# Kernel tuning notes

Measured on AMD Instinct MI355X. Metric: run time of the kernel, lower is better.

## Reference

```python
import jax, jax.numpy as jnp
import numpy as np

B, T, D = 2, 2048, 1024
H = 16
HD = D // H  # 64


def _rope_tables(t_len, hd, dtype=jnp.float32):
    inv_freq = 1.0 / (10000.0 ** (jnp.arange(0, hd, 2, dtype=jnp.float32) / hd))
    freqs = jnp.outer(jnp.arange(t_len, dtype=jnp.float32), inv_freq)  # [T, hd/2]
    emb = jnp.concatenate([freqs, freqs], axis=-1)  # [T, hd]
    return emb.astype(dtype)


def _rotate_half(x):
    x1, x2 = jnp.split(x, 2, axis=-1)
    return jnp.concatenate([-x2, x1], axis=-1)


def setup_inputs() -> dict:
    key = jax.random.key(0)
    k1, k2, k3 = jax.random.split(key, 3)
    x = jax.random.normal(k1, (B, T, D), dtype=jnp.float32)
    w_qkv = jax.random.normal(k2, (D, 3 * D), dtype=jnp.float32) * (D ** -0.5)
    w_out = jax.random.normal(k3, (D, D), dtype=jnp.float32) * (D ** -0.5)
    return {"x": x, "w_qkv": w_qkv, "w_out": w_out}


def reference(x, w_qkv, w_out):
    Bc, Tc, Dc = x.shape
    scale = HD ** -0.5
    qkv = x @ w_qkv  # [B,T,3D]
    q, k, v = jnp.split(qkv, 3, axis=-1)
    # -> [B,H,T,hd]
    q = q.reshape(Bc, Tc, H, HD).transpose(0, 2, 1, 3)
    k = k.reshape(Bc, Tc, H, HD).transpose(0, 2, 1, 3)
    v = v.reshape(Bc, Tc, H, HD).transpose(0, 2, 1, 3)
    emb = _rope_tables(Tc, HD, x.dtype)  # [T,hd]
    cos = jnp.cos(emb)[None, None, :, :]
    sin = jnp.sin(emb)[None, None, :, :]
    q = q * cos + _rotate_half(q) * sin
    k = k * cos + _rotate_half(k) * sin
    attn = jnp.einsum('bhqd,bhkd->bhqk', q, k) * scale  # [B,H,T,T]
    causal = jnp.tril(jnp.ones((Tc, Tc), dtype=bool))
    attn = jnp.where(causal[None, None], attn, -jnp.inf)
    attn = jax.nn.softmax(attn, axis=-1)
    out = jnp.einsum('bhqk,bhkd->bhqd', attn, v)
    out = out.transpose(0, 2, 1, 3).reshape(Bc, Tc, Dc)
    return out @ w_out
```

## Files before the change

### kernel.cpp

```cpp
#include <hip/hip_runtime.h>

#define TSEQ 2048
#define DMODEL 1024
#define NHEAD 16
#define HDIM 64
#define NB 2
#define MROWS 4096
#define NQKV 3072
#define QSCALE 0.1803368801111204f
#define ROPE_C (13.2877123795494f / 32.0f)
#define NEGINF -3.0e38f

using s16x8 = __attribute__((ext_vector_type(8))) short;
using s16x4 = __attribute__((ext_vector_type(4))) short;
using f32x4 = __attribute__((ext_vector_type(4))) float;
using u32x2 = __attribute__((ext_vector_type(2))) unsigned int;

static __device__ __forceinline__ float b2f(unsigned short u) {
  union { unsigned int i; float f; } x; x.i = ((unsigned int)u) << 16; return x.f;
}
static __device__ __forceinline__ unsigned short f2b(float f) {
  unsigned int u = __float_as_uint(f);
  u += 0x7fffu + ((u >> 16) & 1u);
  return (unsigned short)(u >> 16);
}

#if __has_builtin(__builtin_amdgcn_exp2f)
#define EXP2(x) __builtin_amdgcn_exp2f(x)
#else
#define EXP2(x) exp2f(x)
#endif

typedef const __attribute__((address_space(1))) char gchar;
typedef __attribute__((address_space(3))) char lchar;
static __device__ __forceinline__ void gload_lds16(const void* g, void* l) {
  __builtin_amdgcn_global_load_lds((gchar*)g, (lchar*)l, 16, 0, 0);
}

__global__ __launch_bounds__(256) void k_prep(const float* __restrict__ x,
                                              short* __restrict__ xb,
                                              const float* __restrict__ wq,
                                              short* __restrict__ wqT,
                                              const float* __restrict__ wo,
                                              short* __restrict__ woT) {
  __shared__ float tile[32][33];
  const int blk = blockIdx.x;
  const int tid = threadIdx.x;
  if (blk < 4096) {
    const int i = blk * 256 + tid;
    const float4 v = ((const float4*)x)[i];
    s16x4 o;
    o.x = (short)f2b(v.x); o.y = (short)f2b(v.y);
    o.z = (short)f2b(v.z); o.w = (short)f2b(v.w);
    ((s16x4*)xb)[i] = o;
    return;
  }
  const float* in; short* out; int C, bx, by;
  if (blk < 7168) {
    const int l = blk - 4096; in = wq; out = wqT; C = NQKV;
    bx = l % 96; by = l / 96;
  } else {
    const int l = blk - 7168; in = wo; out = woT; C = DMODEL;
    bx = l & 31; by = l >> 5;
  }
  const int tx = tid & 31, ty4 = (tid >> 5) * 4;
#pragma unroll
  for (int i = 0; i < 4; ++i)
    tile[ty4 + i][tx] = in[(by * 32 + ty4 + i) * C + bx * 32 + tx];
  __syncthreads();
#pragma unroll
  for (int i = 0; i < 4; ++i)
    out[(bx * 32 + ty4 + i) * DMODEL + by * 32 + tx] = (short)f2b(tile[tx][ty4 + i]);
}

__global__ __launch_bounds__(256) void k_gemm_qkv(const short* __restrict__ A,
                                                  const short* __restrict__ BT,
                                                  short* __restrict__ Qo,
                                                  short* __restrict__ Ko,
                                                  short* __restrict__ Vt) {
  __shared__ __attribute__((aligned(16))) short As[2][128 * 64];
  __shared__ __attribute__((aligned(16))) short Bs[2][128 * 64];
  const int K = DMODEL;
  const int tid = threadIdx.x;
  const int wave = tid >> 6, lane = tid & 63, quad = lane >> 4, l15 = lane & 15;
  const int wm = (wave >> 1) * 64, wn = (wave & 1) * 64;
  const int m0 = blockIdx.y * 128, n0 = blockIdx.x * 128;
  f32x4 acc[4][4] = {};
  const char* Ab = (const char*)A;
  const char* Bb = (const char*)BT;
  char* AsB = (char*)As;
  char* BsB = (char*)Bs;
  int srow[4], sg[4];
#pragma unroll
  for (int p = 0; p < 4; ++p) {
    const int i = p * 256 + tid;
    srow[p] = i >> 3;
    sg[p] = (i & 7) ^ (srow[p] & 7);
  }
#define QSTAGE(k0v, buf)                                                     \
  do {                                                                       \
    _Pragma("unroll")                                                        \
    for (int p = 0; p < 4; ++p) {                                            \
      const long goA = ((long)(m0 + srow[p]) * K + (k0v)) * 2 + sg[p] * 16;  \
      gload_lds16(Ab + goA, AsB + (buf) * 16384 + p * 4096 + wave * 1024);   \
      const long goB = ((long)(n0 + srow[p]) * K + (k0v)) * 2 + sg[p] * 16;  \
      gload_lds16(Bb + goB, BsB + (buf) * 16384 + p * 4096 + wave * 1024);   \
    }                                                                        \
  } while (0)

  const int nK = K / 64;
  QSTAGE(0, 0);
  for (int kt = 0; kt < nK; ++kt) {
    const int cur = kt & 1;
    if (kt + 1 < nK) {
      QSTAGE((kt + 1) * 64, cur ^ 1);
      asm volatile("s_waitcnt vmcnt(8)" ::: "memory");
    } else {
      asm volatile("s_waitcnt vmcnt(0)" ::: "memory");
    }
    __builtin_amdgcn_s_barrier();
    const char* Ac = AsB + cur * 16384;
    const char* Bc = BsB + cur * 16384;
#pragma unroll
    for (int hf = 0; hf < 2; ++hf) {
      s16x8 af[4], bf[4];
#pragma unroll
      for (int i = 0; i < 4; ++i) {
        const int ra = wm + i * 16 + l15;
        af[i] = *(const s16x8*)(Ac + ra * 128 + (((hf * 4 + quad) ^ (ra & 7)) * 16));
        const int rb = wn + i * 16 + l15;
        bf[i] = *(const s16x8*)(Bc + rb * 128 + (((hf * 4 + quad) ^ (rb & 7)) * 16));
      }
#pragma unroll
      for (int i = 0; i < 4; ++i)
#pragma unroll
        for (int j = 0; j < 4; ++j)
          acc[i][j] = __builtin_amdgcn_mfma_f32_16x16x32_bf16(af[i], bf[j], acc[i][j], 0, 0, 0);
    }
    asm volatile("s_waitcnt lgkmcnt(0)" ::: "memory");
    __builtin_amdgcn_s_barrier();
  }
#undef QSTAGE
  const int colbase = n0 + wn;
  const int region = colbase >> 10;
  const int hh = (colbase & 1023) >> 6;
  const int bq = m0 >> 11;
  const int tbase = (m0 & 2047) + wm;
  char* sw = (char*)As + wave * 8192;
  if (region == 2) {
#pragma unroll
    for (int i = 0; i < 4; ++i)
#pragma unroll
      for (int j = 0; j < 4; ++j) {
        const int d = j * 16 + l15;
        const int t0 = i * 16 + quad * 4;
        s16x4 w;
        w.x = (short)f2b(acc[i][j][0]);
        w.y = (short)f2b(acc[i][j][1]);
        w.z = (short)f2b(acc[i][j][2]);
        w.w = (short)f2b(acc[i][j][3]);
        *(s16x4*)(sw + d * 128 + ((((t0 >> 3) ^ (d & 7))) * 16) + (t0 & 7) * 2) = w;
      }
    short* dstv = Vt + (((long)(bq * NHEAD + hh) * HDIM) << 11);
#pragma unroll
    for (int p = 0; p < 8; ++p) {
      const int linear = p * 64 + lane;
      const int d = linear >> 3, c = linear & 7;
      const s16x8 v = *(const s16x8*)(sw + d * 128 + ((c ^ (d & 7)) * 16));
      *(s16x8*)(dstv + (((long)d) << 11) + tbase + c * 8) = v;
    }
  } else {
    if (region == 1) {
#pragma unroll
      for (int i = 0; i < 4; ++i)
#pragma unroll
        for (int j = 0; j < 2; ++j) {
          const int d = j * 16 + l15;
          const float inv = exp2f(-(float)d * ROPE_C);
#pragma unroll
          for (int r = 0; r < 4; ++r) {
            const int t = tbase + i * 16 + quad * 4 + r;
            float sn, cs;
            __sincosf((float)t * inv, &sn, &cs);
            const float a = acc[i][j][r];
            const float bv = acc[i][j + 2][r];
            acc[i][j][r]     = a * cs - bv * sn;
            acc[i][j + 2][r] = bv * cs + a * sn;
          }
        }
    }
#pragma unroll
    for (int i = 0; i < 4; ++i)
#pragma unroll
      for (int j = 0; j < 4; ++j)
#pragma unroll
        for (int r = 0; r < 4; ++r) {
          const int row = i * 16 + quad * 4 + r;
          const int col = j * 16 + l15;
          *(short*)(sw + row * 128 + ((((col >> 3) ^ (row & 7))) * 16) + (col & 7) * 2)
              = (short)f2b(acc[i][j][r]);
        }
    short* dst = (region ? Ko : Qo) + ((long)(bq * NHEAD + hh) * TSEQ + tbase) * HDIM;
#pragma unroll
    for (int p = 0; p < 8; ++p) {
      const int linear = p * 64 + lane;
      const int r = linear >> 3, c = linear & 7;
      const s16x8 v = *(const s16x8*)(sw + r * 128 + ((c ^ (r & 7)) * 16));
      *(s16x8*)(dst + (long)r * HDIM + c * 8) = v;
    }
  }
}

template <int IM, bool OUT_BF16>
__global__ __launch_bounds__(256) void k_gemm(const short* __restrict__ A,
                                              const short* __restrict__ BT,
                                              void* __restrict__ Cv,
                                              int M, int N, int K) {
  static_assert(IM == 2, "vmcnt literal assumes IM==2 (6 loads/thread)");
  __shared__ __attribute__((aligned(16))) short As[2][IM * 32 * 64];
  __shared__ __attribute__((aligned(16))) short Bs[2][128 * 64];
  const int tid = threadIdx.x;
  const int wave = tid >> 6, lane = tid & 63, quad = lane >> 4, l15 = lane & 15;
  const int wm = (wave >> 1) * (IM * 16), wn = (wave & 1) * 64;
  const int m0 = blockIdx.y * (IM * 32), n0 = blockIdx.x * 128;
  f32x4 acc[IM][4] = {};
  const char* Ab = (const char*)A;
  const char* Bb = (const char*)BT;
  char* AsB = (char*)As;
  char* BsB = (char*)Bs;
  int srow[4], sg[4];
#pragma unroll
  for (int p = 0; p < 4; ++p) {
    const int i = p * 256 + tid;
    srow[p] = i >> 3;
    sg[p] = (i & 7) ^ (srow[p] & 7);
  }
#define GSTAGE(k0v, buf)                                                       \
  do {                                                                         \
    _Pragma("unroll")                                                          \
    for (int p = 0; p < IM; ++p) {                                             \
      const long go = ((long)(m0 + srow[p]) * K + (k0v)) * 2 + sg[p] * 16;     \
      gload_lds16(Ab + go, AsB + (buf) * (IM * 4096) + p * 4096 + wave * 1024);\
    }                                                                          \
    _Pragma("unroll")                                                          \
    for (int p = 0; p < 4; ++p) {                                              \
      const long go = ((long)(n0 + srow[p]) * K + (k0v)) * 2 + sg[p] * 16;     \
      gload_lds16(Bb + go, BsB + (buf) * 16384 + p * 4096 + wave * 1024);      \
    }                                                                          \
  } while (0)

  const int nK = K / 64;
  GSTAGE(0, 0);
  for (int kt = 0; kt < nK; ++kt) {
    const int cur = kt & 1;
    if (kt + 1 < nK) {
      GSTAGE((kt + 1) * 64, cur ^ 1);
      asm volatile("s_waitcnt vmcnt(6)" ::: "memory");
    } else {
      asm volatile("s_waitcnt vmcnt(0)" ::: "memory");
    }
    __builtin_amdgcn_s_barrier();
    const char* Ac = AsB + cur * (IM * 4096);
    const char* Bc = BsB + cur * 16384;
#pragma unroll
    for (int hf = 0; hf < 2; ++hf) {
      s16x8 af[IM], bf[4];
#pragma unroll
      for (int i = 0; i < IM; ++i) {
        const int ra = wm + i * 16 + l15;
        af[i] = *(const s16x8*)(Ac + ra * 128 + (((hf * 4 + quad) ^ (ra & 7)) * 16));
      }
#pragma unroll
      for (int j = 0; j < 4; ++j) {
        const int rb = wn + j * 16 + l15;
        bf[j] = *(const s16x8*)(Bc + rb * 128 + (((hf * 4 + quad) ^ (rb & 7)) * 16));
      }
#pragma unroll
      for (int i = 0; i < IM; ++i)
#pragma unroll
        for (int j = 0; j < 4; ++j)
          acc[i][j] = __builtin_amdgcn_mfma_f32_16x16x32_bf16(af[i], bf[j], acc[i][j], 0, 0, 0);
    }
    asm volatile("s_waitcnt lgkmcnt(0)" ::: "memory");
    __builtin_amdgcn_s_barrier();
  }
#undef GSTAGE
  if (OUT_BF16) {
#pragma unroll
    for (int i = 0; i < IM; ++i) {
      const int row = m0 + wm + i * 16 + quad * 4;
#pragma unroll
      for (int j = 0; j < 4; ++j) {
        const int col = n0 + wn + j * 16 + l15;
#pragma unroll
        for (int r = 0; r < 4; ++r)
          ((short*)Cv)[(long)(row + r) * N + col] = (short)f2b(acc[i][j][r]);
      }
    }
  } else {
    char* sw = (char*)Bs + wave * 8192;
#pragma unroll
    for (int i = 0; i < IM; ++i)
#pragma unroll
      for (int j = 0; j < 4; ++j)
#pragma unroll
        for (int r = 0; r < 4; ++r) {
          const int row = i * 16 + quad * 4 + r;
          const int col = j * 16 + l15;
          *(float*)(sw + row * 256 + ((((col >> 2) ^ (row & 7))) * 16) + (col & 3) * 4)
              = acc[i][j][r];
        }
    float* C = (float*)Cv;
#pragma unroll
    for (int p = 0; p < 8; ++p) {
      const int linear = p * 64 + lane;
      const int r = linear >> 4, c = linear & 15;
      const f32x4 v = *(const f32x4*)(sw + r * 256 + ((c ^ (r & 7)) * 16));
      *(f32x4*)(C + (long)(m0 + wm + r) * N + n0 + wn + c * 4) = v;
    }
  }
}

__global__ __launch_bounds__(512) __attribute__((amdgpu_waves_per_eu(4)))
void k_attn(const short* __restrict__ Qg,
            const short* __restrict__ Kg,
            const short* __restrict__ Vg,
            short* __restrict__ O) {
  __shared__ __attribute__((aligned(16))) short Ks[2][64 * 64];
  __shared__ __attribute__((aligned(16))) short Vs[2][64 * 64];
  __shared__ __attribute__((aligned(16))) short pl[8][16 * 64];
  const int bx = blockIdx.x, by = blockIdx.y;
  const int qi = ((by >> 4) & 1) ? (15 - bx) : bx;
  const int bh = by;
  const int b = bh >> 4, h = bh & 15;
  const int tid = threadIdx.x, wave = tid >> 6, lane = tid & 63;
  const int quad = lane >> 4, l15 = lane & 15;
  const char* Kb = (const char*)(Kg + (long)bh * TSEQ * HDIM);
  const char* Vb = (const char*)(Vg + (long)bh * HDIM * TSEQ);
  const short* Qb = Qg + (long)bh * TSEQ * HDIM;
  const int qr0 = qi * 128 + wave * 16;
  const s16x8 rq0 = *(const s16x8*)&Qb[(qr0 + l15) * HDIM + quad * 8];
  const s16x8 rq1 = *(const s16x8*)&Qb[(qr0 + l15) * HDIM + 32 + quad * 8];
  s16x8 aq0, aq1;
  {
    const float tf = (float)(qr0 + l15);
#pragma unroll
    for (int j = 0; j < 8; ++j) {
      const float inv = exp2f(-(float)(quad * 8 + j) * ROPE_C);
      float sn, cs;
      __sincosf(tf * inv, &sn, &cs);
      sn *= QSCALE; cs *= QSCALE;
      const float q0 = b2f((unsigned short)rq0[j]);
      const float q1 = b2f((unsigned short)rq1[j]);
      aq0[j] = (short)f2b(q0 * cs - q1 * sn);
      aq1[j] = (short)f2b(q1 * cs + q0 * sn);
    }
  }
  s16x8 ones;
#pragma unroll
  for (int j = 0; j < 8; ++j) ones[j] = (short)0x3F80;
  f32x4 o[4] = {};
  f32x4 zs = {};
  const int kr0 = tid >> 3, kg0 = (tid & 7) ^ (kr0 & 7);
  char* KsB = (char*)Ks;
  char* VsB = (char*)Vs;
  char* plwB = (char*)pl + wave * 2048;
  const int ldsw = wave * 1024;

#define STAGE(kjv, buf)                                                     \
  do {                                                                      \
    gload_lds16(Kb + (kjv) * 8192 + (kr0 * 8 + kg0) * 16,                   \
                KsB + (buf) * 8192 + ldsw);                                 \
    gload_lds16(Vb + (kjv) * 128 + kr0 * (TSEQ * 2) + kg0 * 16,             \
                VsB + (buf) * 8192 + ldsw);                                 \
  } while (0)

  STAGE(0, 0);

  const int kjmax = 2 * qi + 1;
  const int kjd = qr0 >> 6;
  for (int kj = 0; kj <= kjmax; ++kj) {
    const int cur = kj & 1;
    if (kj < kjmax) {
      STAGE(kj + 1, cur ^ 1);
      asm volatile("s_waitcnt vmcnt(2)" ::: "memory");
    } else {
      asm volatile("s_waitcnt vmcnt(0)" ::: "memory");
    }
    __builtin_amdgcn_s_barrier();
    if (kj <= kjd) {
      const char* kb = KsB + cur * 8192;
      const char* vb = VsB + cur * 8192;
      f32x4 s[4];
      __builtin_amdgcn_s_setprio(1);
#pragma unroll
      for (int j2 = 0; j2 < 4; ++j2) {
        const int row = j2 * 16 + l15;
        const s16x8 k0 = *(const s16x8*)(kb + row * 128 + ((quad ^ (row & 7)) * 16));
        const s16x8 k1 = *(const s16x8*)(kb + row * 128 + (((4 + quad) ^ (row & 7)) * 16));
        f32x4 z = {};
        z = __builtin_amdgcn_mfma_f32_16x16x32_bf16(k0, aq0, z, 0, 0, 0);
        z = __builtin_amdgcn_mfma_f32_16x16x32_bf16(k1, aq1, z, 0, 0, 0);
        s[j2] = z;
      }
      __builtin_amdgcn_s_setprio(0);
      if (kj == kjd) {
        const int qloc = (qr0 & 63) + l15;
#pragma unroll
        for (int j2 = 0; j2 < 4; ++j2)
#pragma unroll
          for (int r = 0; r < 4; ++r)
            if (j2 * 16 + quad * 4 + r > qloc) s[j2][r] = NEGINF;
      }
#pragma unroll
      for (int j2 = 0; j2 < 4; ++j2) {
        const unsigned int u0 = __float_as_uint(EXP2(s[j2][0])) & 0xffff0000u;
        const unsigned int u1 = __float_as_uint(EXP2(s[j2][1])) & 0xffff0000u;
        const unsigned int u2 = __float_as_uint(EXP2(s[j2][2])) & 0xffff0000u;
        const unsigned int u3 = __float_as_uint(EXP2(s[j2][3])) & 0xffff0000u;
        u32x2 w;
        w.x = (u0 >> 16) | u1;
        w.y = (u2 >> 16) | u3;
        const int t0 = j2 * 16 + quad * 4;
        *(u32x2*)(plwB + l15 * 128 + (((t0 >> 3) ^ (l15 & 7)) * 16) + (quad & 1) * 8) = w;
      }
      const s16x8 bp0 = *(const s16x8*)(plwB + l15 * 128 + ((quad ^ (l15 & 7)) * 16));
      const s16x8 bp1 = *(const s16x8*)(plwB + l15 * 128 + (((4 + quad) ^ (l15 & 7)) * 16));
      __builtin_amdgcn_s_setprio(1);
      zs = __builtin_amdgcn_mfma_f32_16x16x32_bf16(ones, bp0, zs, 0, 0, 0);
      zs = __builtin_amdgcn_mfma_f32_16x16x32_bf16(ones, bp1, zs, 0, 0, 0);
#pragma unroll
      for (int hs = 0; hs < 4; ++hs) {
        const int d = hs * 16 + l15;
        const s16x8 av0 = *(const s16x8*)(vb + d * 128 + ((quad ^ (d & 7)) * 16));
        const s16x8 av1 = *(const s16x8*)(vb + d * 128 + (((4 + quad) ^ (d & 7)) * 16));
        o[hs] = __builtin_amdgcn_mfma_f32_16x16x32_bf16(av0, bp0, o[hs], 0, 0, 0);
        o[hs] = __builtin_amdgcn_mfma_f32_16x16x32_bf16(av1, bp1, o[hs], 0, 0, 0);
      }
      __builtin_amdgcn_s_setprio(0);
    }
    asm volatile("s_waitcnt lgkmcnt(0)" ::: "memory");
    __builtin_amdgcn_s_barrier();
  }
#undef STAGE
  const float rinv = 1.0f / zs[0];
  const int t = qr0 + l15;
  short* Orow = O + (long)(b * TSEQ + t) * DMODEL + h * HDIM + quad * 4;
#pragma unroll
  for (int hs = 0; hs < 4; ++hs) {
    s16x4 w;
    w.x = (short)f2b(o[hs][0] * rinv);
    w.y = (short)f2b(o[hs][1] * rinv);
    w.z = (short)f2b(o[hs][2] * rinv);
    w.w = (short)f2b(o[hs][3] * rinv);
    *(s16x4*)(Orow + hs * 16) = w;
  }
}

extern "C" void kernel_launch(void* const* d_in, const int* in_sizes, int n_in,
                              void* d_out, int out_size, void* d_ws, size_t ws_size,
                              hipStream_t stream) {
  const float* x = (const float*)d_in[0];
  const float* w_qkv = (const float*)d_in[1];
  const float* w_out = (const float*)d_in[2];
  float* out = (float*)d_out;
  char* ws = (char*)d_ws;

  short* xb    = (short*)(ws);
  short* wqkvT = (short*)(ws + (8ll << 20));
  short* woutT = (short*)(ws + (14ll << 20));
  short* Qb    = (short*)(ws + (16ll << 20));
  short* Kb    = (short*)(ws + (24ll << 20));
  short* Vt    = (short*)(ws + (32ll << 20));
  short* Ob    = (short*)(ws + (40ll << 20));

  k_prep<<<dim3(8192), dim3(256), 0, stream>>>(x, xb, w_qkv, wqkvT, w_out, woutT);
  k_gemm_qkv<<<dim3(NQKV / 128, MROWS / 128), dim3(256), 0, stream>>>(
      xb, wqkvT, Qb, Kb, Vt);
  k_attn<<<dim3(TSEQ / 128, NB * NHEAD), dim3(512), 0, stream>>>(Qb, Kb, Vt, Ob);
  k_gemm<2, false><<<dim3(DMODEL / 128, MROWS / 64), dim3(256), 0, stream>>>(
      Ob, woutT, (void*)out, MROWS, DMODEL, DMODEL);
}
```

Measured before the change: 178.5 us.

## Process two query sub-tiles per wave in attention and swizzle GEMM block order

The attention kernel now runs 4 waves of 256 threads instead of 8, and each wave handles 32 query rows as two 16-row sub-tiles. Every K/V fragment read from LDS feeds twice as many MFMAs, and each thread issues twice as many staging loads. Both GEMMs also remap block IDs with an XCD-style swizzle so neighbouring tiles land on the same chiplet and share L2. The costs are higher register pressure from doubled accumulators, fewer waves to hide latency, and no explicit waves_per_eu hint.

```diff
diff --git a/kernel.cpp b/kernel.cpp
--- a/kernel.cpp
+++ b/kernel.cpp
@@ -84,7 +84,10 @@
   const int tid = threadIdx.x;
   const int wave = tid >> 6, lane = tid & 63, quad = lane >> 4, l15 = lane & 15;
   const int wm = (wave >> 1) * 64, wn = (wave & 1) * 64;
-  const int m0 = blockIdx.y * 128, n0 = blockIdx.x * 128;
+  const int bid = blockIdx.y * 24 + blockIdx.x;
+  const int swz = (bid & 7) * 96 + (bid >> 3);
+  const int bx = swz % 24, by = swz / 24;
+  const int m0 = by * 128, n0 = bx * 128;
   f32x4 acc[4][4] = {};
   const char* Ab = (const char*)A;
   const char* Bb = (const char*)BT;
@@ -222,7 +225,11 @@
   const int tid = threadIdx.x;
   const int wave = tid >> 6, lane = tid & 63, quad = lane >> 4, l15 = lane & 15;
   const int wm = (wave >> 1) * (IM * 16), wn = (wave & 1) * 64;
-  const int m0 = blockIdx.y * (IM * 32), n0 = blockIdx.x * 128;
+  const int nwg = gridDim.x * gridDim.y;
+  const int bid = blockIdx.y * gridDim.x + blockIdx.x;
+  const int swz = (bid & 7) * (nwg >> 3) + (bid >> 3);
+  const int bx = swz % gridDim.x, by = swz / gridDim.x;
+  const int m0 = by * (IM * 32), n0 = bx * 128;
   f32x4 acc[IM][4] = {};
   const char* Ab = (const char*)A;
   const char* Bb = (const char*)BT;
@@ -321,14 +328,49 @@
   }
 }
 
-__global__ __launch_bounds__(512) __attribute__((amdgpu_waves_per_eu(4)))
-void k_attn(const short* __restrict__ Qg,
-            const short* __restrict__ Kg,
-            const short* __restrict__ Vg,
-            short* __restrict__ O) {
+static __device__ __forceinline__ void load_rope_q(const short* Qb, int row,
+                                                   int quad, s16x8* a0, s16x8* a1) {
+  const s16x8 r0 = *(const s16x8*)&Qb[row * HDIM + quad * 8];
+  const s16x8 r1 = *(const s16x8*)&Qb[row * HDIM + 32 + quad * 8];
+  const float tf = (float)row;
+  s16x8 o0, o1;
+#pragma unroll
+  for (int j = 0; j < 8; ++j) {
+    const float inv = exp2f(-(float)(quad * 8 + j) * ROPE_C);
+    float sn, cs;
+    __sincosf(tf * inv, &sn, &cs);
+    sn *= QSCALE; cs *= QSCALE;
+    const float q0 = b2f((unsigned short)r0[j]);
+    const float q1 = b2f((unsigned short)r1[j]);
+    o0[j] = (short)f2b(q0 * cs - q1 * sn);
+    o1[j] = (short)f2b(q1 * cs + q0 * sn);
+  }
+  *a0 = o0; *a1 = o1;
+}
+
+static __device__ __forceinline__ void pexp_store(char* plw, const f32x4* s,
+                                                  int quad, int l15) {
+#pragma unroll
+  for (int j2 = 0; j2 < 4; ++j2) {
+    const unsigned int u0 = __float_as_uint(EXP2(s[j2][0])) & 0xffff0000u;
+    const unsigned int u1 = __float_as_uint(EXP2(s[j2][1])) & 0xffff0000u;
+    const unsigned int u2 = __float_as_uint(EXP2(s[j2][2])) & 0xffff0000u;
+    const unsigned int u3 = __float_as_uint(EXP2(s[j2][3])) & 0xffff0000u;
+    u32x2 w;
+    w.x = (u0 >> 16) | u1;
+    w.y = (u2 >> 16) | u3;
+    const int t0 = j2 * 16 + quad * 4;
+    *(u32x2*)(plw + l15 * 128 + (((t0 >> 3) ^ (l15 & 7)) * 16) + (quad & 1) * 8) = w;
+  }
+}
+
+__global__ __launch_bounds__(256) void k_attn(const short* __restrict__ Qg,
+                                              const short* __restrict__ Kg,
+                                              const short* __restrict__ Vg,
+                                              short* __restrict__ O) {
   __shared__ __attribute__((aligned(16))) short Ks[2][64 * 64];
   __shared__ __attribute__((aligned(16))) short Vs[2][64 * 64];
-  __shared__ __attribute__((aligned(16))) short pl[8][16 * 64];
+  __shared__ __attribute__((aligned(16))) short pl[4][2][16 * 64];
   const int bx = blockIdx.x, by = blockIdx.y;
   const int qi = ((by >> 4) & 1) ? (15 - bx) : bx;
   const int bh = by;
@@ -338,41 +380,34 @@
   const char* Kb = (const char*)(Kg + (long)bh * TSEQ * HDIM);
   const char* Vb = (const char*)(Vg + (long)bh * HDIM * TSEQ);
   const short* Qb = Qg + (long)bh * TSEQ * HDIM;
-  const int qr0 = qi * 128 + wave * 16;
-  const s16x8 rq0 = *(const s16x8*)&Qb[(qr0 + l15) * HDIM + quad * 8];
-  const s16x8 rq1 = *(const s16x8*)&Qb[(qr0 + l15) * HDIM + 32 + quad * 8];
-  s16x8 aq0, aq1;
-  {
-    const float tf = (float)(qr0 + l15);
-#pragma unroll
-    for (int j = 0; j < 8; ++j) {
-      const float inv = exp2f(-(float)(quad * 8 + j) * ROPE_C);
-      float sn, cs;
-      __sincosf(tf * inv, &sn, &cs);
-      sn *= QSCALE; cs *= QSCALE;
-      const float q0 = b2f((unsigned short)rq0[j]);
-      const float q1 = b2f((unsigned short)rq1[j]);
-      aq0[j] = (short)f2b(q0 * cs - q1 * sn);
-      aq1[j] = (short)f2b(q1 * cs + q0 * sn);
-    }
-  }
+  const int qr0 = qi * 128 + wave * 32;
+
+  s16x8 aqA0, aqA1, aqB0, aqB1;
+  load_rope_q(Qb, qr0 + l15, quad, &aqA0, &aqA1);
+  load_rope_q(Qb, qr0 + 16 + l15, quad, &aqB0, &aqB1);
+
   s16x8 ones;
 #pragma unroll
   for (int j = 0; j < 8; ++j) ones[j] = (short)0x3F80;
-  f32x4 o[4] = {};
-  f32x4 zs = {};
-  const int kr0 = tid >> 3, kg0 = (tid & 7) ^ (kr0 & 7);
+  f32x4 oA[4] = {}, oB[4] = {}, zsA = {}, zsB = {};
   char* KsB = (char*)Ks;
   char* VsB = (char*)Vs;
-  char* plwB = (char*)pl + wave * 2048;
+  char* plA = (char*)pl + wave * 4096;
+  char* plB = plA + 2048;
+  const int r0 = tid >> 3,        g0 = (tid & 7) ^ (r0 & 7);
+  const int r1 = 32 + (tid >> 3), g1 = (tid & 7) ^ (r1 & 7);
   const int ldsw = wave * 1024;
 
 #define STAGE(kjv, buf)                                                     \
   do {                                                                      \
-    gload_lds16(Kb + (kjv) * 8192 + (kr0 * 8 + kg0) * 16,                   \
+    gload_lds16(Kb + (kjv) * 8192 + (r0 * 8 + g0) * 16,                     \
                 KsB + (buf) * 8192 + ldsw);                                 \
-    gload_lds16(Vb + (kjv) * 128 + kr0 * (TSEQ * 2) + kg0 * 16,             \
+    gload_lds16(Kb + (kjv) * 8192 + (r1 * 8 + g1) * 16,                     \
+                KsB + (buf) * 8192 + 4096 + ldsw);                          \
+    gload_lds16(Vb + (kjv) * 128 + r0 * (TSEQ * 2) + g0 * 16,               \
                 VsB + (buf) * 8192 + ldsw);                                 \
+    gload_lds16(Vb + (kjv) * 128 + r1 * (TSEQ * 2) + g1 * 16,               \
+                VsB + (buf) * 8192 + 4096 + ldsw);                          \
   } while (0)
 
   STAGE(0, 0);
@@ -383,7 +418,7 @@
     const int cur = kj & 1;
     if (kj < kjmax) {
       STAGE(kj + 1, cur ^ 1);
-      asm volatile("s_waitcnt vmcnt(2)" ::: "memory");
+      asm volatile("s_waitcnt vmcnt(4)" ::: "memory");
     } else {
       asm volatile("s_waitcnt vmcnt(0)" ::: "memory");
     }
@@ -391,7 +426,7 @@
     if (kj <= kjd) {
       const char* kb = KsB + cur * 8192;
       const char* vb = VsB + cur * 8192;
-      f32x4 s[4];
+      f32x4 sA[4], sB[4];
       __builtin_amdgcn_s_setprio(1);
 #pragma unroll
       for (int j2 = 0; j2 < 4; ++j2) {
@@ -399,43 +434,46 @@
         const s16x8 k0 = *(const s16x8*)(kb + row * 128 + ((quad ^ (row & 7)) * 16));
         const s16x8 k1 = *(const s16x8*)(kb + row * 128 + (((4 + quad) ^ (row & 7)) * 16));
         f32x4 z = {};
-        z = __builtin_amdgcn_mfma_f32_16x16x32_bf16(k0, aq0, z, 0, 0, 0);
-        z = __builtin_amdgcn_mfma_f32_16x16x32_bf16(k1, aq1, z, 0, 0, 0);
-        s[j2] = z;
+        z = __builtin_amdgcn_mfma_f32_16x16x32_bf16(k0, aqA0, z, 0, 0, 0);
+        z = __builtin_amdgcn_mfma_f32_16x16x32_bf16(k1, aqA1, z, 0, 0, 0);
+        sA[j2] = z;
+        f32x4 y = {};
+        y = __builtin_amdgcn_mfma_f32_16x16x32_bf16(k0, aqB0, y, 0, 0, 0);
+        y = __builtin_amdgcn_mfma_f32_16x16x32_bf16(k1, aqB1, y, 0, 0, 0);
+        sB[j2] = y;
       }
       __builtin_amdgcn_s_setprio(0);
       if (kj == kjd) {
-        const int qloc = (qr0 & 63) + l15;
+        const int qA = (qr0 & 63) + l15;
 #pragma unroll
         for (int j2 = 0; j2 < 4; ++j2)
 #pragma unroll
-          for (int r = 0; r < 4; ++r)
-            if (j2 * 16 + quad * 4 + r > qloc) s[j2][r] = NEGINF;
-      }
-#pragma unroll
-      for (int j2 = 0; j2 < 4; ++j2) {
-        const unsigned int u0 = __float_as_uint(EXP2(s[j2][0])) & 0xffff0000u;
-        const unsigned int u1 = __float_as_uint(EXP2(s[j2][1])) & 0xffff0000u;
-        const unsigned int u2 = __float_as_uint(EXP2(s[j2][2])) & 0xffff0000u;
-        const unsigned int u3 = __float_as_uint(EXP2(s[j2][3])) & 0xffff0000u;
-        u32x2 w;
-        w.x = (u0 >> 16) | u1;
-        w.y = (u2 >> 16) | u3;
-        const int t0 = j2 * 16 + quad * 4;
-        *(u32x2*)(plwB + l15 * 128 + (((t0 >> 3) ^ (l15 & 7)) * 16) + (quad & 1) * 8) = w;
-      }
-      const s16x8 bp0 = *(const s16x8*)(plwB + l15 * 128 + ((quad ^ (l15 & 7)) * 16));
-      const s16x8 bp1 = *(const s16x8*)(plwB + l15 * 128 + (((4 + quad) ^ (l15 & 7)) * 16));
+          for (int r = 0; r < 4; ++r) {
+            const int tl = j2 * 16 + quad * 4 + r;
+            if (tl > qA) sA[j2][r] = NEGINF;
+            if (tl > qA + 16) sB[j2][r] = NEGINF;
+          }
+      }
+      pexp_store(plA, sA, quad, l15);
+      pexp_store(plB, sB, quad, l15);
+      const s16x8 bpA0 = *(const s16x8*)(plA + l15 * 128 + ((quad ^ (l15 & 7)) * 16));
+      const s16x8 bpA1 = *(const s16x8*)(plA + l15 * 128 + (((4 + quad) ^ (l15 & 7)) * 16));
+      const s16x8 bpB0 = *(const s16x8*)(plB + l15 * 128 + ((quad ^ (l15 & 7)) * 16));
+      const s16x8 bpB1 = *(const s16x8*)(plB + l15 * 128 + (((4 + quad) ^ (l15 & 7)) * 16));
       __builtin_amdgcn_s_setprio(1);
-      zs = __builtin_amdgcn_mfma_f32_16x16x32_bf16(ones, bp0, zs, 0, 0, 0);
-      zs = __builtin_amdgcn_mfma_f32_16x16x32_bf16(ones, bp1, zs, 0, 0, 0);
+      zsA = __builtin_amdgcn_mfma_f32_16x16x32_bf16(ones, bpA0, zsA, 0, 0, 0);
+      zsA = __builtin_amdgcn_mfma_f32_16x16x32_bf16(ones, bpA1, zsA, 0, 0, 0);
+      zsB = __builtin_amdgcn_mfma_f32_16x16x32_bf16(ones, bpB0, zsB, 0, 0, 0);
+      zsB = __builtin_amdgcn_mfma_f32_16x16x32_bf16(ones, bpB1, zsB, 0, 0, 0);
 #pragma unroll
       for (int hs = 0; hs < 4; ++hs) {
         const int d = hs * 16 + l15;
         const s16x8 av0 = *(const s16x8*)(vb + d * 128 + ((quad ^ (d & 7)) * 16));
         const s16x8 av1 = *(const s16x8*)(vb + d * 128 + (((4 + quad) ^ (d & 7)) * 16));
-        o[hs] = __builtin_amdgcn_mfma_f32_16x16x32_bf16(av0, bp0, o[hs], 0, 0, 0);
-        o[hs] = __builtin_amdgcn_mfma_f32_16x16x32_bf16(av1, bp1, o[hs], 0, 0, 0);
+        oA[hs] = __builtin_amdgcn_mfma_f32_16x16x32_bf16(av0, bpA0, oA[hs], 0, 0, 0);
+        oA[hs] = __builtin_amdgcn_mfma_f32_16x16x32_bf16(av1, bpA1, oA[hs], 0, 0, 0);
+        oB[hs] = __builtin_amdgcn_mfma_f32_16x16x32_bf16(av0, bpB0, oB[hs], 0, 0, 0);
+        oB[hs] = __builtin_amdgcn_mfma_f32_16x16x32_bf16(av1, bpB1, oB[hs], 0, 0, 0);
       }
       __builtin_amdgcn_s_setprio(0);
     }
@@ -443,17 +481,33 @@
     __builtin_amdgcn_s_barrier();
   }
 #undef STAGE
-  const float rinv = 1.0f / zs[0];
-  const int t = qr0 + l15;
-  short* Orow = O + (long)(b * TSEQ + t) * DMODEL + h * HDIM + quad * 4;
-#pragma unroll
-  for (int hs = 0; hs < 4; ++hs) {
-    s16x4 w;
-    w.x = (short)f2b(o[hs][0] * rinv);
-    w.y = (short)f2b(o[hs][1] * rinv);
-    w.z = (short)f2b(o[hs][2] * rinv);
-    w.w = (short)f2b(o[hs][3] * rinv);
-    *(s16x4*)(Orow + hs * 16) = w;
+  const float rA = 1.0f / zsA[0];
+  const float rB = 1.0f / zsB[0];
+  {
+    const int t = qr0 + l15;
+    short* Orow = O + (long)(b * TSEQ + t) * DMODEL + h * HDIM + quad * 4;
+#pragma unroll
+    for (int hs = 0; hs < 4; ++hs) {
+      s16x4 w;
+      w.x = (short)f2b(oA[hs][0] * rA);
+      w.y = (short)f2b(oA[hs][1] * rA);
+      w.z = (short)f2b(oA[hs][2] * rA);
+      w.w = (short)f2b(oA[hs][3] * rA);
+      *(s16x4*)(Orow + hs * 16) = w;
+    }
+  }
+  {
+    const int t = qr0 + 16 + l15;
+    short* Orow = O + (long)(b * TSEQ + t) * DMODEL + h * HDIM + quad * 4;
+#pragma unroll
+    for (int hs = 0; hs < 4; ++hs) {
+      s16x4 w;
+      w.x = (short)f2b(oB[hs][0] * rB);
+      w.y = (short)f2b(oB[hs][1] * rB);
+      w.z = (short)f2b(oB[hs][2] * rB);
+      w.w = (short)f2b(oB[hs][3] * rB);
+      *(s16x4*)(Orow + hs * 16) = w;
+    }
   }
 }
 
@@ -477,7 +531,7 @@
   k_prep<<<dim3(8192), dim3(256), 0, stream>>>(x, xb, w_qkv, wqkvT, w_out, woutT);
   k_gemm_qkv<<<dim3(NQKV / 128, MROWS / 128), dim3(256), 0, stream>>>(
       xb, wqkvT, Qb, Kb, Vt);
-  k_attn<<<dim3(TSEQ / 128, NB * NHEAD), dim3(512), 0, stream>>>(Qb, Kb, Vt, Ob);
+  k_attn<<<dim3(TSEQ / 128, NB * NHEAD), dim3(256), 0, stream>>>(Qb, Kb, Vt, Ob);
   k_gemm<2, false><<<dim3(DMODEL / 128, MROWS / 64), dim3(256), 0, stream>>>(
       Ob, woutT, (void*)out, MROWS, DMODEL, DMODEL);
 }
```

After: 187.8 us. 5.2% more time.

## Stage QKV GEMM tiles through registers, single LDS buffer, and XCD-swizzle workgroups

Applied to the files above, without the earlier changes.

The QKV GEMM drops the double-buffered direct global-to-LDS loads. It prefetches the next K-tile into registers, then writes it to a single swizzled LDS buffer after the MFMA work, adding an extra barrier per iteration. This halves LDS use to allow more occupancy, but adds register pressure and an extra sync. Both GEMM kernels also remap block IDs with a stride-8 swizzle so neighbouring tiles land on the same XCD, aiming for better L2 reuse.

```diff
diff --git a/kernel.cpp b/kernel.cpp
--- a/kernel.cpp
+++ b/kernel.cpp
@@ -78,58 +78,62 @@
                                                   short* __restrict__ Qo,
                                                   short* __restrict__ Ko,
                                                   short* __restrict__ Vt) {
-  __shared__ __attribute__((aligned(16))) short As[2][128 * 64];
-  __shared__ __attribute__((aligned(16))) short Bs[2][128 * 64];
+  __shared__ __attribute__((aligned(16))) short As[128 * 64];
+  __shared__ __attribute__((aligned(16))) short Bs[128 * 64];
   const int K = DMODEL;
   const int tid = threadIdx.x;
   const int wave = tid >> 6, lane = tid & 63, quad = lane >> 4, l15 = lane & 15;
   const int wm = (wave >> 1) * 64, wn = (wave & 1) * 64;
-  const int m0 = blockIdx.y * 128, n0 = blockIdx.x * 128;
+  const int bid = blockIdx.y * 24 + blockIdx.x;
+  const int swz = (bid & 7) * 96 + (bid >> 3);
+  const int bx = swz % 24, by = swz / 24;
+  const int m0 = by * 128, n0 = bx * 128;
   f32x4 acc[4][4] = {};
   const char* Ab = (const char*)A;
   const char* Bb = (const char*)BT;
   char* AsB = (char*)As;
   char* BsB = (char*)Bs;
-  int srow[4], sg[4];
+  int srow[4], scg[4], ssw[4];
 #pragma unroll
   for (int p = 0; p < 4; ++p) {
     const int i = p * 256 + tid;
     srow[p] = i >> 3;
-    sg[p] = (i & 7) ^ (srow[p] & 7);
-  }
-#define QSTAGE(k0v, buf)                                                     \
-  do {                                                                       \
-    _Pragma("unroll")                                                        \
-    for (int p = 0; p < 4; ++p) {                                            \
-      const long goA = ((long)(m0 + srow[p]) * K + (k0v)) * 2 + sg[p] * 16;  \
-      gload_lds16(Ab + goA, AsB + (buf) * 16384 + p * 4096 + wave * 1024);   \
-      const long goB = ((long)(n0 + srow[p]) * K + (k0v)) * 2 + sg[p] * 16;  \
-      gload_lds16(Bb + goB, BsB + (buf) * 16384 + p * 4096 + wave * 1024);   \
-    }                                                                        \
+    scg[p] = i & 7;
+    ssw[p] = scg[p] ^ (srow[p] & 7);
+  }
+#define QLOAD(k0v)                                                            \
+  do {                                                                        \
+    _Pragma("unroll")                                                         \
+    for (int p = 0; p < 4; ++p) {                                             \
+      ra[p] = *(const f32x4*)(Ab + ((long)(m0 + srow[p]) * K + (k0v)) * 2 + scg[p] * 16); \
+      rb[p] = *(const f32x4*)(Bb + ((long)(n0 + srow[p]) * K + (k0v)) * 2 + scg[p] * 16); \
+    }                                                                         \
   } while (0)
-
+#define QWRITE()                                                              \
+  do {                                                                        \
+    _Pragma("unroll")                                                         \
+    for (int p = 0; p < 4; ++p) {                                             \
+      *(f32x4*)(AsB + srow[p] * 128 + ssw[p] * 16) = ra[p];                   \
+      *(f32x4*)(BsB + srow[p] * 128 + ssw[p] * 16) = rb[p];                   \
+    }                                                                         \
+  } while (0)
+
+  f32x4 ra[4], rb[4];
   const int nK = K / 64;
-  QSTAGE(0, 0);
+  QLOAD(0);
+  QWRITE();
+  __syncthreads();
   for (int kt = 0; kt < nK; ++kt) {
-    const int cur = kt & 1;
-    if (kt + 1 < nK) {
-      QSTAGE((kt + 1) * 64, cur ^ 1);
-      asm volatile("s_waitcnt vmcnt(8)" ::: "memory");
-    } else {
-      asm volatile("s_waitcnt vmcnt(0)" ::: "memory");
-    }
-    __builtin_amdgcn_s_barrier();
-    const char* Ac = AsB + cur * 16384;
-    const char* Bc = BsB + cur * 16384;
+    if (kt + 1 < nK) QLOAD((kt + 1) * 64);
 #pragma unroll
     for (int hf = 0; hf < 2; ++hf) {
       s16x8 af[4], bf[4];
 #pragma unroll
       for (int i = 0; i < 4; ++i) {
-        const int ra = wm + i * 16 + l15;
-        af[i] = *(const s16x8*)(Ac + ra * 128 + (((hf * 4 + quad) ^ (ra & 7)) * 16));
-        const int rb = wn + i * 16 + l15;
-        bf[i] = *(const s16x8*)(Bc + rb * 128 + (((hf * 4 + quad) ^ (rb & 7)) * 16));
+        const int rowa = wm + i * 16 + l15;
+        af[i] = *(const s16x8*)(AsB + rowa * 128 + (((hf * 4 + quad) ^ (rowa & 7)) * 16));
+        const int rowb = wn + i * 16 + l15;
+        bf[i] = *(const s16x8*)(BsB + rowb * 128 + (((hf * 4 + quad) ^ (rowb & 7)) * 16));
       }
 #pragma unroll
       for (int i = 0; i < 4; ++i)
@@ -139,14 +143,20 @@
     }
     asm volatile("s_waitcnt lgkmcnt(0)" ::: "memory");
     __builtin_amdgcn_s_barrier();
-  }
-#undef QSTAGE
+    if (kt + 1 < nK) {
+      QWRITE();
+      asm volatile("s_waitcnt lgkmcnt(0)" ::: "memory");
+      __builtin_amdgcn_s_barrier();
+    }
+  }
+#undef QLOAD
+#undef QWRITE
   const int colbase = n0 + wn;
   const int region = colbase >> 10;
   const int hh = (colbase & 1023) >> 6;
   const int bq = m0 >> 11;
   const int tbase = (m0 & 2047) + wm;
-  char* sw = (char*)As + wave * 8192;
+  char* sw = (wave < 2) ? (AsB + wave * 8192) : (BsB + (wave - 2) * 8192);
   if (region == 2) {
 #pragma unroll
     for (int i = 0; i < 4; ++i)
@@ -222,7 +232,11 @@
   const int tid = threadIdx.x;
   const int wave = tid >> 6, lane = tid & 63, quad = lane >> 4, l15 = lane & 15;
   const int wm = (wave >> 1) * (IM * 16), wn = (wave & 1) * 64;
-  const int m0 = blockIdx.y * (IM * 32), n0 = blockIdx.x * 128;
+  const int nwg = gridDim.x * gridDim.y;
+  const int bid = blockIdx.y * gridDim.x + blockIdx.x;
+  const int swz = (bid & 7) * (nwg >> 3) + (bid >> 3);
+  const int bx = swz % gridDim.x, by = swz / gridDim.x;
+  const int m0 = by * (IM * 32), n0 = bx * 128;
   f32x4 acc[IM][4] = {};
   const char* Ab = (const char*)A;
   const char* Bb = (const char*)BT;
@@ -267,13 +281,13 @@
       s16x8 af[IM], bf[4];
 #pragma unroll
       for (int i = 0; i < IM; ++i) {
-        const int ra = wm + i * 16 + l15;
-        af[i] = *(const s16x8*)(Ac + ra * 128 + (((hf * 4 + quad) ^ (ra & 7)) * 16));
+        const int rowa = wm + i * 16 + l15;
+        af[i] = *(const s16x8*)(Ac + rowa * 128 + (((hf * 4 + quad) ^ (rowa & 7)) * 16));
       }
 #pragma unroll
       for (int j = 0; j < 4; ++j) {
-        const int rb = wn + j * 16 + l15;
-        bf[j] = *(const s16x8*)(Bc + rb * 128 + (((hf * 4 + quad) ^ (rb & 7)) * 16));
+        const int rowb = wn + j * 16 + l15;
+        bf[j] = *(const s16x8*)(Bc + rowb * 128 + (((hf * 4 + quad) ^ (rowb & 7)) * 16));
       }
 #pragma unroll
       for (int i = 0; i < IM; ++i)
```

Result: no change. 176.2 us (median of 2 runs) (-1.3%).

## Enlarge QKV GEMM to 256x256 tiles with 8 waves, phased staging, and block swizzle

Applied to the files above, without the earlier changes.

Rewrites the QKV projection GEMM to use 256x256 output tiles with 512 threads (8 waves, 2x4 layout). Each wave now holds 128x64 of the output, and global-to-LDS staging for the next K-tile is split into four phases interleaved with MFMA work, using s_setprio to favour the matrix ops. A grouped block-index swizzle is added to both the QKV GEMM and the output-projection GEMM to improve L2 reuse. The larger tile cuts redundant global loads per FLOP, at the cost of 128KB of LDS, more accumulator registers, more barriers per K step, and only 192 blocks for the QKV GEMM.

```diff
diff --git a/kernel.cpp b/kernel.cpp
--- a/kernel.cpp
+++ b/kernel.cpp
@@ -73,140 +73,176 @@
     out[(bx * 32 + ty4 + i) * DMODEL + by * 32 + tx] = (short)f2b(tile[tx][ty4 + i]);
 }
 
-__global__ __launch_bounds__(256) void k_gemm_qkv(const short* __restrict__ A,
-                                                  const short* __restrict__ BT,
-                                                  short* __restrict__ Qo,
-                                                  short* __restrict__ Ko,
-                                                  short* __restrict__ Vt) {
-  __shared__ __attribute__((aligned(16))) short As[2][128 * 64];
-  __shared__ __attribute__((aligned(16))) short Bs[2][128 * 64];
+__global__ __launch_bounds__(512, 2) void k_gemm_qkv(const short* __restrict__ A,
+                                                     const short* __restrict__ BT,
+                                                     short* __restrict__ Qo,
+                                                     short* __restrict__ Ko,
+                                                     short* __restrict__ Vt) {
+  __shared__ __attribute__((aligned(16))) short L[2][2][2][128 * 64];
   const int K = DMODEL;
   const int tid = threadIdx.x;
   const int wave = tid >> 6, lane = tid & 63, quad = lane >> 4, l15 = lane & 15;
-  const int wm = (wave >> 1) * 64, wn = (wave & 1) * 64;
-  const int m0 = blockIdx.y * 128, n0 = blockIdx.x * 128;
-  f32x4 acc[4][4] = {};
-  const char* Ab = (const char*)A;
-  const char* Bb = (const char*)BT;
-  char* AsB = (char*)As;
-  char* BsB = (char*)Bs;
-  int srow[4], sg[4];
-#pragma unroll
-  for (int p = 0; p < 4; ++p) {
-    const int i = p * 256 + tid;
-    srow[p] = i >> 3;
-    sg[p] = (i & 7) ^ (srow[p] & 7);
-  }
-#define QSTAGE(k0v, buf)                                                     \
-  do {                                                                       \
-    _Pragma("unroll")                                                        \
-    for (int p = 0; p < 4; ++p) {                                            \
-      const long goA = ((long)(m0 + srow[p]) * K + (k0v)) * 2 + sg[p] * 16;  \
-      gload_lds16(Ab + goA, AsB + (buf) * 16384 + p * 4096 + wave * 1024);   \
-      const long goB = ((long)(n0 + srow[p]) * K + (k0v)) * 2 + sg[p] * 16;  \
-      gload_lds16(Bb + goB, BsB + (buf) * 16384 + p * 4096 + wave * 1024);   \
-    }                                                                        \
+  const int wr = wave >> 2, wc = wave & 3;
+  const int bid = blockIdx.y * 12 + blockIdx.x;
+  const int swz = (bid & 7) * 24 + (bid >> 3);
+  const int bx = swz % 12, by = swz / 12;
+  const int m0 = by * 256, n0 = bx * 256;
+  f32x4 acc[8][4] = {};
+  char* Lb = (char*)L;
+  const int r0 = tid >> 3, pc = tid & 7;
+  const int sc0 = pc ^ (r0 & 7);
+  const int r1 = 64 + r0;
+  const int sc1 = pc ^ (r1 & 7);
+#define HBASE(buf, ab, h) (Lb + (((buf) * 4 + (ab) * 2 + (h)) * 16384))
+#define STAGE_HT(kt1, ab, h)                                                   \
+  do {                                                                         \
+    const short* src_ = (ab) ? BT : A;                                         \
+    const int rowb_ = ((ab) ? n0 : m0) + (h) * 128;                            \
+    const long o0_ = ((long)(rowb_ + r0) * K + (kt1) * 64) * 2 + sc0 * 16;     \
+    const long o1_ = ((long)(rowb_ + r1) * K + (kt1) * 64) * 2 + sc1 * 16;     \
+    char* db_ = HBASE((kt1) & 1, ab, h) + wave * 1024;                         \
+    gload_lds16((const char*)src_ + o0_, db_);                                 \
+    gload_lds16((const char*)src_ + o1_, db_ + 8192);                          \
   } while (0)
 
-  const int nK = K / 64;
-  QSTAGE(0, 0);
-  for (int kt = 0; kt < nK; ++kt) {
+  const int nT = K / 64;
+  STAGE_HT(0, 0, 0); STAGE_HT(0, 0, 1); STAGE_HT(0, 1, 0); STAGE_HT(0, 1, 1);
+
+  const int rbb = (wc & 1) * 64;
+  for (int kt = 0; kt < nT; ++kt) {
     const int cur = kt & 1;
-    if (kt + 1 < nK) {
-      QSTAGE((kt + 1) * 64, cur ^ 1);
-      asm volatile("s_waitcnt vmcnt(8)" ::: "memory");
+    const char* Ah = HBASE(cur, 0, wr);
+    const char* Bh = HBASE(cur, 1, wc >> 1);
+    s16x8 bf[4][2];
+#pragma unroll
+    for (int ph = 0; ph < 4; ++ph) {
+      s16x8 af[2][2];
+      if (ph == 0) {
+        if (kt + 1 < nT) {
+          STAGE_HT(kt + 1, 0, 0);
+          asm volatile("s_waitcnt vmcnt(2)" ::: "memory");
+        } else {
+          asm volatile("s_waitcnt vmcnt(0)" ::: "memory");
+        }
+        __builtin_amdgcn_s_barrier();
+#pragma unroll
+        for (int g = 0; g < 4; ++g)
+#pragma unroll
+          for (int kh = 0; kh < 2; ++kh) {
+            const int rb = rbb + g * 16 + l15;
+            bf[g][kh] = *(const s16x8*)(Bh + rb * 128 +
+                                        (((kh * 4 + quad) ^ (l15 & 7)) * 16));
+          }
+#pragma unroll
+        for (int f2 = 0; f2 < 2; ++f2)
+#pragma unroll
+          for (int kh = 0; kh < 2; ++kh) {
+            const int ra = (ph * 2 + f2) * 16 + l15;
+            af[f2][kh] = *(const s16x8*)(Ah + ra * 128 +
+                                         (((kh * 4 + quad) ^ (l15 & 7)) * 16));
+          }
+      } else {
+#pragma unroll
+        for (int f2 = 0; f2 < 2; ++f2)
+#pragma unroll
+          for (int kh = 0; kh < 2; ++kh) {
+            const int ra = (ph * 2 + f2) * 16 + l15;
+            af[f2][kh] = *(const s16x8*)(Ah + ra * 128 +
+                                         (((kh * 4 + quad) ^ (l15 & 7)) * 16));
+          }
+        if (kt + 1 < nT) {
+          if (ph == 1)      STAGE_HT(kt + 1, 0, 1);
+          else if (ph == 2) STAGE_HT(kt + 1, 1, 0);
+          else              STAGE_HT(kt + 1, 1, 1);
+        }
+        __builtin_amdgcn_s_barrier();
+      }
+      asm volatile("s_waitcnt lgkmcnt(0)" ::: "memory");
+      __builtin_amdgcn_s_setprio(1);
+#pragma unroll
+      for (int f2 = 0; f2 < 2; ++f2)
+#pragma unroll
+        for (int g = 0; g < 4; ++g) {
+          acc[ph * 2 + f2][g] = __builtin_amdgcn_mfma_f32_16x16x32_bf16(
+              af[f2][0], bf[g][0], acc[ph * 2 + f2][g], 0, 0, 0);
+          acc[ph * 2 + f2][g] = __builtin_amdgcn_mfma_f32_16x16x32_bf16(
+              af[f2][1], bf[g][1], acc[ph * 2 + f2][g], 0, 0, 0);
+        }
+      __builtin_amdgcn_s_setprio(0);
+      __builtin_amdgcn_s_barrier();
+    }
+  }
+#undef STAGE_HT
+#undef HBASE
+  const int colhead = n0 + wc * 64;
+  const int region = colhead >> 10;
+  const int hh = (colhead & 1023) >> 6;
+  const int bq = m0 >> 11;
+  char* sw = Lb + wave * 8192;
+  if (region == 1) {
+#pragma unroll
+    for (int f = 0; f < 8; ++f)
+#pragma unroll
+      for (int g = 0; g < 2; ++g) {
+        const int d = g * 16 + l15;
+        const float inv = exp2f(-(float)d * ROPE_C);
+#pragma unroll
+        for (int r = 0; r < 4; ++r) {
+          const int t = (m0 & 2047) + wr * 128 + f * 16 + quad * 4 + r;
+          float sn, cs;
+          __sincosf((float)t * inv, &sn, &cs);
+          const float a = acc[f][g][r];
+          const float bv = acc[f][g + 2][r];
+          acc[f][g][r]     = a * cs - bv * sn;
+          acc[f][g + 2][r] = bv * cs + a * sn;
+        }
+      }
+  }
+#pragma unroll
+  for (int P = 0; P < 2; ++P) {
+    const int tb = (m0 & 2047) + wr * 128 + P * 64;
+    if (region == 2) {
+#pragma unroll
+      for (int i2 = 0; i2 < 4; ++i2)
+#pragma unroll
+        for (int g = 0; g < 4; ++g) {
+          const int d = g * 16 + l15;
+          const int t0 = i2 * 16 + quad * 4;
+          s16x4 w;
+          w.x = (short)f2b(acc[P * 4 + i2][g][0]);
+          w.y = (short)f2b(acc[P * 4 + i2][g][1]);
+          w.z = (short)f2b(acc[P * 4 + i2][g][2]);
+          w.w = (short)f2b(acc[P * 4 + i2][g][3]);
+          *(s16x4*)(sw + d * 128 + ((((t0 >> 3) ^ (d & 7))) * 16) + (t0 & 7) * 2) = w;
+        }
+      short* dstv = Vt + (((long)(bq * NHEAD + hh) * HDIM) << 11);
+#pragma unroll
+      for (int p = 0; p < 8; ++p) {
+        const int linear = p * 64 + lane;
+        const int d = linear >> 3, c = linear & 7;
+        const s16x8 v = *(const s16x8*)(sw + d * 128 + ((c ^ (d & 7)) * 16));
+        *(s16x8*)(dstv + (((long)d) << 11) + tb + c * 8) = v;
+      }
     } else {
-      asm volatile("s_waitcnt vmcnt(0)" ::: "memory");
-    }
-    __builtin_amdgcn_s_barrier();
-    const char* Ac = AsB + cur * 16384;
-    const char* Bc = BsB + cur * 16384;
-#pragma unroll
-    for (int hf = 0; hf < 2; ++hf) {
-      s16x8 af[4], bf[4];
-#pragma unroll
-      for (int i = 0; i < 4; ++i) {
-        const int ra = wm + i * 16 + l15;
-        af[i] = *(const s16x8*)(Ac + ra * 128 + (((hf * 4 + quad) ^ (ra & 7)) * 16));
-        const int rb = wn + i * 16 + l15;
-        bf[i] = *(const s16x8*)(Bc + rb * 128 + (((hf * 4 + quad) ^ (rb & 7)) * 16));
-      }
-#pragma unroll
-      for (int i = 0; i < 4; ++i)
-#pragma unroll
-        for (int j = 0; j < 4; ++j)
-          acc[i][j] = __builtin_amdgcn_mfma_f32_16x16x32_bf16(af[i], bf[j], acc[i][j], 0, 0, 0);
-    }
-    asm volatile("s_waitcnt lgkmcnt(0)" ::: "memory");
-    __builtin_amdgcn_s_barrier();
-  }
-#undef QSTAGE
-  const int colbase = n0 + wn;
-  const int region = colbase >> 10;
-  const int hh = (colbase & 1023) >> 6;
-  const int bq = m0 >> 11;
-  const int tbase = (m0 & 2047) + wm;
-  char* sw = (char*)As + wave * 8192;
-  if (region == 2) {
-#pragma unroll
-    for (int i = 0; i < 4; ++i)
-#pragma unroll
-      for (int j = 0; j < 4; ++j) {
-        const int d = j * 16 + l15;
-        const int t0 = i * 16 + quad * 4;
-        s16x4 w;
-        w.x = (short)f2b(acc[i][j][0]);
-        w.y = (short)f2b(acc[i][j][1]);
-        w.z = (short)f2b(acc[i][j][2]);
-        w.w = (short)f2b(acc[i][j][3]);
-        *(s16x4*)(sw + d * 128 + ((((t0 >> 3) ^ (d & 7))) * 16) + (t0 & 7) * 2) = w;
-      }
-    short* dstv = Vt + (((long)(bq * NHEAD + hh) * HDIM) << 11);
-#pragma unroll
-    for (int p = 0; p < 8; ++p) {
-      const int linear = p * 64 + lane;
-      const int d = linear >> 3, c = linear & 7;
-      const s16x8 v = *(const s16x8*)(sw + d * 128 + ((c ^ (d & 7)) * 16));
-      *(s16x8*)(dstv + (((long)d) << 11) + tbase + c * 8) = v;
-    }
-  } else {
-    if (region == 1) {
-#pragma unroll
-      for (int i = 0; i < 4; ++i)
-#pragma unroll
-        for (int j = 0; j < 2; ++j) {
-          const int d = j * 16 + l15;
-          const float inv = exp2f(-(float)d * ROPE_C);
+#pragma unroll
+      for (int i2 = 0; i2 < 4; ++i2)
+#pragma unroll
+        for (int g = 0; g < 4; ++g)
 #pragma unroll
           for (int r = 0; r < 4; ++r) {
-            const int t = tbase + i * 16 + quad * 4 + r;
-            float sn, cs;
-            __sincosf((float)t * inv, &sn, &cs);
-            const float a = acc[i][j][r];
-            const float bv = acc[i][j + 2][r];
-            acc[i][j][r]     = a * cs - bv * sn;
-            acc[i][j + 2][r] = bv * cs + a * sn;
+            const int row = i2 * 16 + quad * 4 + r;
+            const int col = g * 16 + l15;
+            *(short*)(sw + row * 128 + ((((col >> 3) ^ (row & 7))) * 16) + (col & 7) * 2)
+                = (short)f2b(acc[P * 4 + i2][g][r]);
           }
-        }
-    }
-#pragma unroll
-    for (int i = 0; i < 4; ++i)
-#pragma unroll
-      for (int j = 0; j < 4; ++j)
-#pragma unroll
-        for (int r = 0; r < 4; ++r) {
-          const int row = i * 16 + quad * 4 + r;
-          const int col = j * 16 + l15;
-          *(short*)(sw + row * 128 + ((((col >> 3) ^ (row & 7))) * 16) + (col & 7) * 2)
-              = (short)f2b(acc[i][j][r]);
-        }
-    short* dst = (region ? Ko : Qo) + ((long)(bq * NHEAD + hh) * TSEQ + tbase) * HDIM;
-#pragma unroll
-    for (int p = 0; p < 8; ++p) {
-      const int linear = p * 64 + lane;
-      const int r = linear >> 3, c = linear & 7;
-      const s16x8 v = *(const s16x8*)(sw + r * 128 + ((c ^ (r & 7)) * 16));
-      *(s16x8*)(dst + (long)r * HDIM + c * 8) = v;
+      short* dst = (region ? Ko : Qo) + ((long)(bq * NHEAD + hh) * TSEQ + tb) * HDIM;
+#pragma unroll
+      for (int p = 0; p < 8; ++p) {
+        const int linear = p * 64 + lane;
+        const int rr = linear >> 3, c = linear & 7;
+        const s16x8 v = *(const s16x8*)(sw + rr * 128 + ((c ^ (rr & 7)) * 16));
+        *(s16x8*)(dst + (long)rr * HDIM + c * 8) = v;
+      }
     }
   }
 }
@@ -222,7 +258,11 @@
   const int tid = threadIdx.x;
   const int wave = tid >> 6, lane = tid & 63, quad = lane >> 4, l15 = lane & 15;
   const int wm = (wave >> 1) * (IM * 16), wn = (wave & 1) * 64;
-  const int m0 = blockIdx.y * (IM * 32), n0 = blockIdx.x * 128;
+  const int nwg = gridDim.x * gridDim.y;
+  const int bid = blockIdx.y * gridDim.x + blockIdx.x;
+  const int swz = (bid & 7) * (nwg >> 3) + (bid >> 3);
+  const int bx = swz % gridDim.x, by = swz / gridDim.x;
+  const int m0 = by * (IM * 32), n0 = bx * 128;
   f32x4 acc[IM][4] = {};
   const char* Ab = (const char*)A;
   const char* Bb = (const char*)BT;
@@ -267,13 +307,13 @@
       s16x8 af[IM], bf[4];
 #pragma unroll
       for (int i = 0; i < IM; ++i) {
-        const int ra = wm + i * 16 + l15;
-        af[i] = *(const s16x8*)(Ac + ra * 128 + (((hf * 4 + quad) ^ (ra & 7)) * 16));
+        const int rowa = wm + i * 16 + l15;
+        af[i] = *(const s16x8*)(Ac + rowa * 128 + (((hf * 4 + quad) ^ (rowa & 7)) * 16));
       }
 #pragma unroll
       for (int j = 0; j < 4; ++j) {
-        const int rb = wn + j * 16 + l15;
-        bf[j] = *(const s16x8*)(Bc + rb * 128 + (((hf * 4 + quad) ^ (rb & 7)) * 16));
+        const int rowb = wn + j * 16 + l15;
+        bf[j] = *(const s16x8*)(Bc + rowb * 128 + (((hf * 4 + quad) ^ (rowb & 7)) * 16));
       }
 #pragma unroll
       for (int i = 0; i < IM; ++i)
@@ -475,7 +515,7 @@
   short* Ob    = (short*)(ws + (40ll << 20));
 
   k_prep<<<dim3(8192), dim3(256), 0, stream>>>(x, xb, w_qkv, wqkvT, w_out, woutT);
-  k_gemm_qkv<<<dim3(NQKV / 128, MROWS / 128), dim3(256), 0, stream>>>(
+  k_gemm_qkv<<<dim3(NQKV / 256, MROWS / 256), dim3(512), 0, stream>>>(
       xb, wqkvT, Qb, Kb, Vt);
   k_attn<<<dim3(TSEQ / 128, NB * NHEAD), dim3(512), 0, stream>>>(Qb, Kb, Vt, Ob);
   k_gemm<2, false><<<dim3(DMODEL / 128, MROWS / 64), dim3(256), 0, stream>>>(
```

After: 168.8 us. 1.06x faster.
